# Optimization experiments

Hardware: AMD Instinct MI355X
Metric: run time of the kernel (lower is better)

The kernel has to match this reference:

```python
import jax, jax.numpy as jnp
import numpy as np

N_UU_LAYERS = 2
N_II_LAYERS = 2
ALPHA = 0.5
BETA = 0.5


def _sym_norm(edge_index, n):
    # PyG gcn_norm without self loops: norm = deg^-1/2[row] * deg^-1/2[col]
    row, col = edge_index[0], edge_index[1]
    deg = jax.ops.segment_sum(jnp.ones(row.shape, jnp.float32), col, num_segments=n)
    dinv = jnp.where(deg > 0, jax.lax.rsqrt(jnp.maximum(deg, 1e-12)), 0.0)
    return dinv[row] * dinv[col]


def _propagate(x, edge_index, norm, n):
    # gather from source, weight by norm, scatter-sum into target
    row, col = edge_index[0], edge_index[1]
    return jax.ops.segment_sum(norm[:, None] * x[row], col, num_segments=n)


def setup_inputs() -> dict:
    key = jax.random.key(0)
    ks = jax.random.split(key, 16)
    U, I, D, R, S = 50000, 50000, 64, 5, 2
    E_REL, E_SIM, B = 1000000, 1600000, 8192
    sc = 0.1  # xavier-ish scale for d=64
    return {
        "Gu": jax.random.normal(ks[0], (U, D), jnp.float32) * sc,
        "Gi": jax.random.normal(ks[1], (I, D), jnp.float32) * sc,
        "Gus": jax.random.normal(ks[2], (U, D), jnp.float32) * sc,
        "Gis": jax.random.normal(ks[3], (I, D), jnp.float32) * sc,
        "W_conv": jax.random.normal(ks[4], (R, D, D), jnp.float32) * sc,
        "W_dense": jax.random.normal(ks[5], (D, D), jnp.float32) * sc,
        "P": jax.random.normal(ks[6], (S, D, D), jnp.float32) * sc,
        "A": jax.random.uniform(ks[7], (R, S), jnp.float32),
        "relations": jnp.arange(1, R + 1, dtype=jnp.float32),
        "edge_index_rel": jax.random.randint(ks[8], (R, 2, E_REL), 0, U + I, jnp.int32),
        "edge_index_uu": jax.random.randint(ks[9], (2, E_SIM), 0, U, jnp.int32),
        "edge_index_ii": jax.random.randint(ks[10], (2, E_SIM), 0, I, jnp.int32),
        "user": jax.random.randint(ks[11], (B,), 0, U, jnp.int32),
        "item": jax.random.randint(ks[12], (B,), 0, I, jnp.int32),
    }


def reference(Gu, Gi, Gus, Gis, W_conv, W_dense, P, A, relations,
              edge_index_rel, edge_index_uu, edge_index_ii, user, item):
    U, I = Gu.shape[0], Gi.shape[0]
    N = U + I
    R = W_conv.shape[0]

    # LGConv stacks on user-user and item-item similarity graphs
    norm_uu = _sym_norm(edge_index_uu, U)
    gus = Gus
    for _ in range(N_UU_LAYERS):
        gus = _propagate(gus, edge_index_uu, norm_uu, U)
    norm_ii = _sym_norm(edge_index_ii, I)
    gis = Gis
    for _ in range(N_II_LAYERS):
        gis = _propagate(gis, edge_index_ii, norm_ii, I)

    # Per-relation GCNConv (1 layer, linear-then-aggregate, ReLU), sum accumulation
    x0 = jnp.concatenate([Gu, Gi], axis=0)  # [N, D]
    acc = jnp.zeros((N, W_conv.shape[2]), x0.dtype)
    for r in range(R):
        ei = edge_index_rel[r]
        norm = _sym_norm(ei, N)
        xr = x0 @ W_conv[r]
        xr = jax.nn.relu(_propagate(xr, ei, norm, N))
        acc = acc + xr

    emb = acc @ W_dense  # dense layer, no bias; dropout p=0
    zu, zi = emb[:U], emb[U:]

    # batch gather and blend with similarity-propagated embeddings
    gu = (1.0 - ALPHA) * zu[user] + ALPHA * gus[user]
    gi_b = (1.0 - BETA) * zi[item] + BETA * gis[item]

    # basis-weighted bilinear scoring per relation
    Q = jnp.einsum('rs,sde->rde', A, P)             # [R, D, D]
    pui = jnp.einsum('bd,rde,be->br', gu, Q, gi_b)  # [B, R]
    xui = jnp.sum(relations * jax.nn.softmax(pui, axis=1), axis=1)
    return (xui, pui)
```

## Files before the change

kernel.cpp:

```cpp
#include <hip/hip_runtime.h>
#include <hip/hip_bf16.h>

#define DD 64
#define C_REL 40
#define C_SIM 80

static inline int cdiv(long long a, long long b) { return (int)((a + b - 1) / b); }


__global__ void k_scatter_pad(const int* __restrict__ row, const int* __restrict__ col, int E,
                              int* __restrict__ cnt, int* __restrict__ edp, int C) {
    int e = blockIdx.x * blockDim.x + threadIdx.x;
    if (e >= E) return;
    int r = row[e], c = col[e];
    int pos = atomicAdd(&cnt[c], 1);
    if (pos < C) edp[(size_t)c * C + pos] = r;
}

__global__ void k_scatter_rel(const int* __restrict__ row, const int* __restrict__ col, int E,
                              int* __restrict__ cnt, int* __restrict__ edp, int C,
                              const unsigned char* __restrict__ sel) {
    int e = blockIdx.x * blockDim.x + threadIdx.x;
    if (e >= E) return;
    int r = row[e], c = col[e];
    int pos = atomicAdd(&cnt[c], 1);
    if (sel[c] && pos < C) edp[(size_t)c * C + pos] = r;
}

__global__ void k_mark(unsigned char* __restrict__ sel, const int* __restrict__ user,
                       const int* __restrict__ item, int B, int U) {
    int t = blockIdx.x * blockDim.x + threadIdx.x;
    if (t >= 2 * B) return;
    int node = (t < B) ? user[t] : (U + item[t - B]);
    sel[node] = 1;
}

__global__ void k_dinv_i(const int* __restrict__ cnt, float* __restrict__ dinv, int n) {
    int i = blockIdx.x * blockDim.x + threadIdx.x;
    if (i < n) { int d = cnt[i]; dinv[i] = d > 0 ? rsqrtf((float)d) : 0.f; }
}


__global__ __launch_bounds__(256) void k_gather_pad(const float* __restrict__ src, float* __restrict__ dst,
                                                    const int* __restrict__ edp, const int* __restrict__ cnt,
                                                    const float* __restrict__ dinv, int C, int nNodes) {
    int t = blockIdx.x * blockDim.x + threadIdx.x;
    int node = t >> 4;
    if (node >= nNodes) return;
    int k4 = (t & 15) << 2;
    int deg = cnt[node]; if (deg > C) deg = C;
    float dc = dinv[node];
    const int* lst = edp + (size_t)node * C;
    float4 acc = make_float4(0.f, 0.f, 0.f, 0.f);
    for (int e = 0; e < deg; ++e) {
        int rs = lst[e];
        float nn = dc * dinv[rs];
        float4 v = *(const float4*)(src + (size_t)rs * DD + k4);
        acc.x += nn * v.x; acc.y += nn * v.y; acc.z += nn * v.z; acc.w += nn * v.w;
    }
    *(float4*)(dst + (size_t)node * DD + k4) = acc;
}

__global__ __launch_bounds__(256) void k_gather_sel_sim(const float* __restrict__ src, float* __restrict__ dst,
                                                        const int* __restrict__ edp, const int* __restrict__ cnt,
                                                        const float* __restrict__ dinv, int C,
                                                        const int* __restrict__ idx, int B) {
    int t = blockIdx.x * blockDim.x + threadIdx.x;
    int j = t >> 4;
    if (j >= B) return;
    int k4 = (t & 15) << 2;
    int node = idx[j];
    int deg = cnt[node]; if (deg > C) deg = C;
    float dc = dinv[node];
    const int* lst = edp + (size_t)node * C;
    float4 acc = make_float4(0.f, 0.f, 0.f, 0.f);
    for (int e = 0; e < deg; ++e) {
        int rs = lst[e];
        float nn = dc * dinv[rs];
        float4 v = *(const float4*)(src + (size_t)rs * DD + k4);
        acc.x += nn * v.x; acc.y += nn * v.y; acc.z += nn * v.z; acc.w += nn * v.w;
    }
    *(float4*)(dst + (size_t)j * DD + k4) = acc;
}

__global__ __launch_bounds__(256) void k_gather_x0_rel(const float* __restrict__ Gu, const float* __restrict__ Gi,
                                                       int U, float* __restrict__ TMP,
                                                       const int* __restrict__ edp, const int* __restrict__ cnt,
                                                       int C, const int* __restrict__ user,
                                                       const int* __restrict__ item, int B) {
    int t = blockIdx.x * blockDim.x + threadIdx.x;
    int j = t >> 4;
    if (j >= 2 * B) return;
    int k4 = (t & 15) << 2;
    int node = (j < B) ? user[j] : (U + item[j - B]);
    int cn = cnt[node];
    int deg = cn > C ? C : cn;
    float dc = cn > 0 ? rsqrtf((float)cn) : 0.f;
    const int* lst = edp + (size_t)node * C;
    float4 acc = make_float4(0.f, 0.f, 0.f, 0.f);
    for (int e = 0; e < deg; ++e) {
        int rs = lst[e];
        int cr = cnt[rs];
        float nn = dc * (cr > 0 ? rsqrtf((float)cr) : 0.f);
        const float* srow = (rs < U) ? (Gu + (size_t)rs * DD) : (Gi + (size_t)(rs - U) * DD);
        float4 v = *(const float4*)(srow + k4);
        acc.x += nn * v.x; acc.y += nn * v.y; acc.z += nn * v.z; acc.w += nn * v.w;
    }
    *(float4*)(TMP + (size_t)j * DD + k4) = acc;
}


template <bool RELU_ACC>
__global__ __launch_bounds__(256) void k_matmul64t(const float* __restrict__ X, const float* __restrict__ W,
                                                   float* __restrict__ out, int Nrows) {
    __shared__ float Wl[64 * 64];
    int tid = threadIdx.x;
    for (int t = tid; t < 1024; t += 256) ((float4*)Wl)[t] = ((const float4*)W)[t];
    __syncthreads();
    int row = blockIdx.x * 64 + (tid >> 2);
    if (row >= Nrows) return;
    const float* xs = X + (size_t)row * DD;
    int j0 = (tid & 3) << 4;
    float acc[16];
#pragma unroll
    for (int j = 0; j < 16; ++j) acc[j] = 0.f;
#pragma unroll 4
    for (int k = 0; k < 64; k += 4) {
        float4 xv = *(const float4*)(xs + k);
        const float* w0 = Wl + k * 64 + j0;
#pragma unroll
        for (int j = 0; j < 16; ++j) acc[j] += xv.x * w0[j];
#pragma unroll
        for (int j = 0; j < 16; ++j) acc[j] += xv.y * w0[64 + j];
#pragma unroll
        for (int j = 0; j < 16; ++j) acc[j] += xv.z * w0[128 + j];
#pragma unroll
        for (int j = 0; j < 16; ++j) acc[j] += xv.w * w0[192 + j];
    }
    float* o = out + (size_t)row * DD + j0;
    if (RELU_ACC) {
#pragma unroll
        for (int j = 0; j < 4; ++j) {
            float4 cur = ((float4*)o)[j];
            cur.x += fmaxf(acc[4 * j + 0], 0.f);
            cur.y += fmaxf(acc[4 * j + 1], 0.f);
            cur.z += fmaxf(acc[4 * j + 2], 0.f);
            cur.w += fmaxf(acc[4 * j + 3], 0.f);
            ((float4*)o)[j] = cur;
        }
    } else {
#pragma unroll
        for (int j = 0; j < 4; ++j)
            ((float4*)o)[j] = make_float4(acc[4 * j], acc[4 * j + 1], acc[4 * j + 2], acc[4 * j + 3]);
    }
}

__global__ void k_blend(const float* __restrict__ gus_sel, const float* __restrict__ gis_sel,
                        const float* __restrict__ EMB, float* __restrict__ gu, float* __restrict__ gi,
                        int B) {
    int t = blockIdx.x * blockDim.x + threadIdx.x;
    if (t >= 2 * B * 16) return;
    int j = t >> 4, k = t & 15;
    float4 e = ((const float4*)(EMB + (size_t)j * DD))[k];
    if (j < B) {
        float4 s = ((const float4*)(gus_sel + (size_t)j * DD))[k];
        ((float4*)(gu + (size_t)j * DD))[k] =
            make_float4(0.5f * (s.x + e.x), 0.5f * (s.y + e.y), 0.5f * (s.z + e.z), 0.5f * (s.w + e.w));
    } else {
        int jj = j - B;
        float4 s = ((const float4*)(gis_sel + (size_t)jj * DD))[k];
        ((float4*)(gi + (size_t)jj * DD))[k] =
            make_float4(0.5f * (s.x + e.x), 0.5f * (s.y + e.y), 0.5f * (s.z + e.z), 0.5f * (s.w + e.w));
    }
}

__global__ void k_build_Q(const float* __restrict__ A, const float* __restrict__ P,
                          float* __restrict__ Q, int R, int S) {
    int t = blockIdx.x * blockDim.x + threadIdx.x;
    if (t >= R * 4096) return;
    int r = t / 4096, de = t % 4096;
    float acc = 0.f;
    for (int s = 0; s < S; ++s) acc += A[r * S + s] * P[(size_t)s * 4096 + de];
    Q[t] = acc;
}

__global__ __launch_bounds__(256) void k_pui2(const float* __restrict__ gu, const float* __restrict__ gi,
                                              const float* __restrict__ Q, float* __restrict__ pout,
                                              int B, int R) {
    int wid = (int)(((long long)blockIdx.x * blockDim.x + threadIdx.x) >> 6);
    int lane = threadIdx.x & 63;
    if (wid >= B * R) return;
    int b = wid / R, r = wid % R;
    const float* Qr = Q + (size_t)r * 4096;
    float gu_l = gu[(size_t)b * DD + lane];
    float gi_l = gi[(size_t)b * DD + lane];
    float acc = 0.f;
#pragma unroll 8
    for (int d = 0; d < 64; ++d) {
        float gud = __shfl(gu_l, d, 64);
        acc += gud * Qr[d * 64 + lane];
    }
    acc *= gi_l;
#pragma unroll
    for (int off = 32; off > 0; off >>= 1) acc += __shfl_down(acc, off, 64);
    if (lane == 0) pout[wid] = acc;
}

__global__ void k_softmax_out(const float* __restrict__ pui, const float* __restrict__ rel,
                              float* __restrict__ xui, int B, int R) {
    int b = blockIdx.x * blockDim.x + threadIdx.x;
    if (b >= B) return;
    float m = -1e30f;
    for (int r = 0; r < R; ++r) m = fmaxf(m, pui[(size_t)b * R + r]);
    float se = 0.f, sw = 0.f;
    for (int r = 0; r < R; ++r) {
        float e = expf(pui[(size_t)b * R + r] - m);
        se += e; sw += rel[r] * e;
    }
    xui[b] = sw / se;
}

extern "C" void kernel_launch(void* const* d_in, const int* in_sizes, int n_in,
                              void* d_out, int out_size, void* d_ws, size_t ws_size,
                              hipStream_t stream) {
    const float* Gu      = (const float*)d_in[0];
    const float* Gi      = (const float*)d_in[1];
    const float* Gus     = (const float*)d_in[2];
    const float* Gis     = (const float*)d_in[3];
    const float* W_conv  = (const float*)d_in[4];
    const float* W_dense = (const float*)d_in[5];
    const float* P       = (const float*)d_in[6];
    const float* A       = (const float*)d_in[7];
    const float* rel     = (const float*)d_in[8];
    const int*   ei_rel  = (const int*)d_in[9];
    const int*   ei_uu   = (const int*)d_in[10];
    const int*   ei_ii   = (const int*)d_in[11];
    const int*   user    = (const int*)d_in[12];
    const int*   item    = (const int*)d_in[13];

    const int U = in_sizes[0] / DD;
    const int I = in_sizes[1] / DD;
    const int N = U + I;
    const int R = in_sizes[8];
    const int S = in_sizes[6] / 4096;
    const int E_REL = in_sizes[9] / (2 * R);
    const int E_SIM = in_sizes[10] / 2;
    const int B = in_sizes[12];
    const size_t RN = (size_t)R * N;

    size_t edpElems = (size_t)U * C_SIM;
    if ((size_t)I * C_SIM > edpElems) edpElems = (size_t)I * C_SIM;
    if ((size_t)N * C_REL > edpElems) edpElems = (size_t)N * C_REL;
    edpElems = (edpElems + 3) & ~(size_t)3;

    int maxUI = U > I ? U : I;

    char* p = (char*)d_ws;
    int*   edp     = (int*)p;   p += edpElems * 4;
    int*   cnt     = (int*)p;   p += RN * 4;
    float* dinv    = (float*)p; p += (size_t)(U + I) * 4;
    unsigned char* sel = (unsigned char*)p; p += ((size_t)N + 15) & ~(size_t)15;
    float* gus_sel = (float*)p; p += (size_t)B * DD * 4;
    float* gis_sel = (float*)p; p += (size_t)B * DD * 4;
    float* ACC     = (float*)p; p += (size_t)2 * B * DD * 4;
    float* TMP     = (float*)p; p += (size_t)2 * B * DD * 4;
    float* EMB     = (float*)p; p += (size_t)2 * B * DD * 4;
    float* gu      = (float*)p; p += (size_t)B * DD * 4;
    float* gi      = (float*)p; p += (size_t)B * DD * 4;
    float* Q       = (float*)p; p += (size_t)R * 4096 * 4;
    float* BIG0    = (float*)p; p += (size_t)maxUI * DD * 4;

    float* xui = (float*)d_out;
    float* pui = (float*)d_out + B;

    const int BT = 256;

    hipMemsetAsync(cnt, 0, (size_t)(U + I) * 4, stream);
    k_scatter_pad<<<cdiv(E_SIM, BT), BT, 0, stream>>>(ei_uu, ei_uu + E_SIM, E_SIM, cnt, edp, C_SIM);
    k_dinv_i<<<cdiv(U, BT), BT, 0, stream>>>(cnt, dinv, U);
    k_gather_pad<<<cdiv((long long)U * 16, BT), BT, 0, stream>>>(Gus, BIG0, edp, cnt, dinv, C_SIM, U);
    k_gather_sel_sim<<<cdiv((long long)B * 16, BT), BT, 0, stream>>>(BIG0, gus_sel, edp, cnt, dinv, C_SIM, user, B);
    k_scatter_pad<<<cdiv(E_SIM, BT), BT, 0, stream>>>(ei_ii, ei_ii + E_SIM, E_SIM, cnt + U, edp, C_SIM);
    k_dinv_i<<<cdiv(I, BT), BT, 0, stream>>>(cnt + U, dinv + U, I);
    k_gather_pad<<<cdiv((long long)I * 16, BT), BT, 0, stream>>>(Gis, BIG0, edp, cnt + U, dinv + U, C_SIM, I);
    k_gather_sel_sim<<<cdiv((long long)B * 16, BT), BT, 0, stream>>>(BIG0, gis_sel, edp, cnt + U, dinv + U, C_SIM, item, B);

    hipMemsetAsync(cnt, 0, RN * 4, stream);
    hipMemsetAsync(sel, 0, (size_t)N, stream);
    hipMemsetAsync(ACC, 0, (size_t)2 * B * DD * 4, stream);
    k_mark<<<cdiv(2 * B, BT), BT, 0, stream>>>(sel, user, item, B, U);
    for (int r = 0; r < R; ++r) {
        const int* rrow = ei_rel + (size_t)r * 2 * E_REL;
        const int* rcol = rrow + E_REL;
        k_scatter_rel<<<cdiv(E_REL, BT), BT, 0, stream>>>(rrow, rcol, E_REL, cnt + (size_t)r * N, edp, C_REL, sel);
        k_gather_x0_rel<<<cdiv((long long)2 * B * 16, BT), BT, 0, stream>>>(Gu, Gi, U, TMP, edp,
                                                                            cnt + (size_t)r * N, C_REL,
                                                                            user, item, B);
        k_matmul64t<true><<<cdiv(2 * B, 64), BT, 0, stream>>>(TMP, W_conv + (size_t)r * 4096, ACC, 2 * B);
    }

    k_matmul64t<false><<<cdiv(2 * B, 64), BT, 0, stream>>>(ACC, W_dense, EMB, 2 * B);
    k_blend<<<cdiv((long long)2 * B * 16, BT), BT, 0, stream>>>(gus_sel, gis_sel, EMB, gu, gi, B);

    k_build_Q<<<cdiv((long long)R * 4096, BT), BT, 0, stream>>>(A, P, Q, R, S);
    k_pui2<<<cdiv((long long)B * R * 64, BT), BT, 0, stream>>>(gu, gi, Q, pui, B, R);
    k_softmax_out<<<cdiv(B, BT), BT, 0, stream>>>(pui, rel, xui, B, R);
}
```

Baseline: 958.1 us.

## Merge user/item similarity passes, use 16-bit padded adjacency, split relation histogram

```diff
diff --git a/kernel.cpp b/kernel.cpp
--- a/kernel.cpp
+++ b/kernel.cpp
@@ -7,24 +7,112 @@
 
 static inline int cdiv(long long a, long long b) { return (int)((a + b - 1) / b); }
 
-
-__global__ void k_scatter_pad(const int* __restrict__ row, const int* __restrict__ col, int E,
-                              int* __restrict__ cnt, int* __restrict__ edp, int C) {
-    int e = blockIdx.x * blockDim.x + threadIdx.x;
-    if (e >= E) return;
-    int r = row[e], c = col[e];
-    int pos = atomicAdd(&cnt[c], 1);
-    if (pos < C) edp[(size_t)c * C + pos] = r;
-}
-
-__global__ void k_scatter_rel(const int* __restrict__ row, const int* __restrict__ col, int E,
-                              int* __restrict__ cnt, int* __restrict__ edp, int C,
-                              const unsigned char* __restrict__ sel) {
-    int e = blockIdx.x * blockDim.x + threadIdx.x;
-    if (e >= E) return;
-    int r = row[e], c = col[e];
-    int pos = atomicAdd(&cnt[c], 1);
-    if (sel[c] && pos < C) edp[(size_t)c * C + pos] = r;
+__global__ void k_scatter_sim16(const int* __restrict__ rowU, const int* __restrict__ colU,
+                                const int* __restrict__ rowI, const int* __restrict__ colI,
+                                int E, int U, int* __restrict__ cnt,
+                                unsigned short* __restrict__ edpU, unsigned short* __restrict__ edpI) {
+    long long t = (long long)blockIdx.x * blockDim.x + threadIdx.x;
+    if (t >= 2LL * E) return;
+    if (t < E) {
+        int r = rowU[t], c = colU[t];
+        int pos = atomicAdd(&cnt[c], 1);
+        if (pos < C_SIM) edpU[(size_t)c * C_SIM + pos] = (unsigned short)r;
+    } else {
+        int e = (int)(t - E);
+        int r = rowI[e], c = colI[e];
+        int pos = atomicAdd(&cnt[U + c], 1);
+        if (pos < C_SIM) edpI[(size_t)c * C_SIM + pos] = (unsigned short)r;
+    }
+}
+
+__global__ void k_dinv_i(const int* __restrict__ cnt, float* __restrict__ dinv, int n) {
+    int i = blockIdx.x * blockDim.x + threadIdx.x;
+    if (i < n) { int d = cnt[i]; dinv[i] = d > 0 ? rsqrtf((float)d) : 0.f; }
+}
+
+__global__ __launch_bounds__(256) void k_gather_sim1(const float* __restrict__ Gus, const float* __restrict__ Gis,
+                                                     int U, int UI, float* __restrict__ H1,
+                                                     const unsigned short* __restrict__ edpU,
+                                                     const unsigned short* __restrict__ edpI,
+                                                     const int* __restrict__ cnt, const float* __restrict__ dinv) {
+    int t = blockIdx.x * blockDim.x + threadIdx.x;
+    int node = t >> 4;
+    if (node >= UI) return;
+    int k4 = (t & 15) << 2;
+    int deg = cnt[node]; if (deg > C_SIM) deg = C_SIM;
+    float dc = dinv[node];
+    float4 acc = make_float4(0.f, 0.f, 0.f, 0.f);
+    if (node < U) {
+        const unsigned short* lst = edpU + (size_t)node * C_SIM;
+        for (int e = 0; e < deg; ++e) {
+            int rs = lst[e];
+            float nn = dc * dinv[rs];
+            float4 v = *(const float4*)(Gus + (size_t)rs * DD + k4);
+            acc.x += nn * v.x; acc.y += nn * v.y; acc.z += nn * v.z; acc.w += nn * v.w;
+        }
+    } else {
+        int loc = node - U;
+        const unsigned short* lst = edpI + (size_t)loc * C_SIM;
+        for (int e = 0; e < deg; ++e) {
+            int rs = lst[e];
+            float nn = dc * dinv[U + rs];
+            float4 v = *(const float4*)(Gis + (size_t)rs * DD + k4);
+            acc.x += nn * v.x; acc.y += nn * v.y; acc.z += nn * v.z; acc.w += nn * v.w;
+        }
+    }
+    *(float4*)(H1 + (size_t)node * DD + k4) = acc;
+}
+
+__global__ __launch_bounds__(256) void k_gather_sim2(const float* __restrict__ H1, int U,
+                                                     float* __restrict__ SEL2,
+                                                     const unsigned short* __restrict__ edpU,
+                                                     const unsigned short* __restrict__ edpI,
+                                                     const int* __restrict__ cnt, const float* __restrict__ dinv,
+                                                     const int* __restrict__ user, const int* __restrict__ item,
+                                                     int B) {
+    int t = blockIdx.x * blockDim.x + threadIdx.x;
+    int j = t >> 4;
+    if (j >= 2 * B) return;
+    int k4 = (t & 15) << 2;
+    float4 acc = make_float4(0.f, 0.f, 0.f, 0.f);
+    if (j < B) {
+        int node = user[j];
+        int deg = cnt[node]; if (deg > C_SIM) deg = C_SIM;
+        float dc = dinv[node];
+        const unsigned short* lst = edpU + (size_t)node * C_SIM;
+        for (int e = 0; e < deg; ++e) {
+            int rs = lst[e];
+            float nn = dc * dinv[rs];
+            float4 v = *(const float4*)(H1 + (size_t)rs * DD + k4);
+            acc.x += nn * v.x; acc.y += nn * v.y; acc.z += nn * v.z; acc.w += nn * v.w;
+        }
+    } else {
+        int loc = item[j - B];
+        int deg = cnt[U + loc]; if (deg > C_SIM) deg = C_SIM;
+        float dc = dinv[U + loc];
+        const unsigned short* lst = edpI + (size_t)loc * C_SIM;
+        for (int e = 0; e < deg; ++e) {
+            int rs = lst[e];
+            float nn = dc * dinv[U + rs];
+            float4 v = *(const float4*)(H1 + (size_t)(U + rs) * DD + k4);
+            acc.x += nn * v.x; acc.y += nn * v.y; acc.z += nn * v.z; acc.w += nn * v.w;
+        }
+    }
+    *(float4*)(SEL2 + (size_t)j * DD + k4) = acc;
+}
+
+
+__global__ void k_hist_rel(const int* __restrict__ ei_rel, int E, int N, int R,
+                           int* __restrict__ cntRel) {
+    long long total = (long long)R * E;
+    long long t = (long long)blockIdx.x * blockDim.x + threadIdx.x;
+    long long stride = (long long)gridDim.x * blockDim.x;
+    for (; t < total; t += stride) {
+        int r = (int)(t / E);
+        int e = (int)(t - (long long)r * E);
+        int c = ei_rel[(size_t)r * 2 * E + E + e];
+        atomicAdd(&cntRel[(size_t)r * N + c], 1);
+    }
 }
 
 __global__ void k_mark(unsigned char* __restrict__ sel, const int* __restrict__ user,
@@ -35,58 +123,21 @@
     sel[node] = 1;
 }
 
-__global__ void k_dinv_i(const int* __restrict__ cnt, float* __restrict__ dinv, int n) {
-    int i = blockIdx.x * blockDim.x + threadIdx.x;
-    if (i < n) { int d = cnt[i]; dinv[i] = d > 0 ? rsqrtf((float)d) : 0.f; }
-}
-
-
-__global__ __launch_bounds__(256) void k_gather_pad(const float* __restrict__ src, float* __restrict__ dst,
-                                                    const int* __restrict__ edp, const int* __restrict__ cnt,
-                                                    const float* __restrict__ dinv, int C, int nNodes) {
-    int t = blockIdx.x * blockDim.x + threadIdx.x;
-    int node = t >> 4;
-    if (node >= nNodes) return;
-    int k4 = (t & 15) << 2;
-    int deg = cnt[node]; if (deg > C) deg = C;
-    float dc = dinv[node];
-    const int* lst = edp + (size_t)node * C;
-    float4 acc = make_float4(0.f, 0.f, 0.f, 0.f);
-    for (int e = 0; e < deg; ++e) {
-        int rs = lst[e];
-        float nn = dc * dinv[rs];
-        float4 v = *(const float4*)(src + (size_t)rs * DD + k4);
-        acc.x += nn * v.x; acc.y += nn * v.y; acc.z += nn * v.z; acc.w += nn * v.w;
-    }
-    *(float4*)(dst + (size_t)node * DD + k4) = acc;
-}
-
-__global__ __launch_bounds__(256) void k_gather_sel_sim(const float* __restrict__ src, float* __restrict__ dst,
-                                                        const int* __restrict__ edp, const int* __restrict__ cnt,
-                                                        const float* __restrict__ dinv, int C,
-                                                        const int* __restrict__ idx, int B) {
-    int t = blockIdx.x * blockDim.x + threadIdx.x;
-    int j = t >> 4;
-    if (j >= B) return;
-    int k4 = (t & 15) << 2;
-    int node = idx[j];
-    int deg = cnt[node]; if (deg > C) deg = C;
-    float dc = dinv[node];
-    const int* lst = edp + (size_t)node * C;
-    float4 acc = make_float4(0.f, 0.f, 0.f, 0.f);
-    for (int e = 0; e < deg; ++e) {
-        int rs = lst[e];
-        float nn = dc * dinv[rs];
-        float4 v = *(const float4*)(src + (size_t)rs * DD + k4);
-        acc.x += nn * v.x; acc.y += nn * v.y; acc.z += nn * v.z; acc.w += nn * v.w;
-    }
-    *(float4*)(dst + (size_t)j * DD + k4) = acc;
+__global__ void k_scatter_rel_f(const int* __restrict__ row, const int* __restrict__ col, int E,
+                                const unsigned char* __restrict__ sel, int* __restrict__ cur,
+                                int* __restrict__ edp) {
+    int e = blockIdx.x * blockDim.x + threadIdx.x;
+    if (e >= E) return;
+    int c = col[e];
+    if (!sel[c]) return;
+    int pos = atomicAdd(&cur[c], 1);
+    if (pos < C_REL) edp[(size_t)c * C_REL + pos] = row[e];
 }
 
 __global__ __launch_bounds__(256) void k_gather_x0_rel(const float* __restrict__ Gu, const float* __restrict__ Gi,
                                                        int U, float* __restrict__ TMP,
                                                        const int* __restrict__ edp, const int* __restrict__ cnt,
-                                                       int C, const int* __restrict__ user,
+                                                       const int* __restrict__ user,
                                                        const int* __restrict__ item, int B) {
     int t = blockIdx.x * blockDim.x + threadIdx.x;
     int j = t >> 4;
@@ -94,9 +145,9 @@
     int k4 = (t & 15) << 2;
     int node = (j < B) ? user[j] : (U + item[j - B]);
     int cn = cnt[node];
-    int deg = cn > C ? C : cn;
+    int deg = cn > C_REL ? C_REL : cn;
     float dc = cn > 0 ? rsqrtf((float)cn) : 0.f;
-    const int* lst = edp + (size_t)node * C;
+    const int* lst = edp + (size_t)node * C_REL;
     float4 acc = make_float4(0.f, 0.f, 0.f, 0.f);
     for (int e = 0; e < deg; ++e) {
         int rs = lst[e];
@@ -155,23 +206,16 @@
     }
 }
 
-__global__ void k_blend(const float* __restrict__ gus_sel, const float* __restrict__ gis_sel,
-                        const float* __restrict__ EMB, float* __restrict__ gu, float* __restrict__ gi,
-                        int B) {
+__global__ void k_blend(const float* __restrict__ SEL2, const float* __restrict__ EMB,
+                        float* __restrict__ gu, float* __restrict__ gi, int B) {
     int t = blockIdx.x * blockDim.x + threadIdx.x;
     if (t >= 2 * B * 16) return;
     int j = t >> 4, k = t & 15;
     float4 e = ((const float4*)(EMB + (size_t)j * DD))[k];
-    if (j < B) {
-        float4 s = ((const float4*)(gus_sel + (size_t)j * DD))[k];
-        ((float4*)(gu + (size_t)j * DD))[k] =
-            make_float4(0.5f * (s.x + e.x), 0.5f * (s.y + e.y), 0.5f * (s.z + e.z), 0.5f * (s.w + e.w));
-    } else {
-        int jj = j - B;
-        float4 s = ((const float4*)(gis_sel + (size_t)jj * DD))[k];
-        ((float4*)(gi + (size_t)jj * DD))[k] =
-            make_float4(0.5f * (s.x + e.x), 0.5f * (s.y + e.y), 0.5f * (s.z + e.z), 0.5f * (s.w + e.w));
-    }
+    float4 s = ((const float4*)(SEL2 + (size_t)j * DD))[k];
+    float4 o = make_float4(0.5f * (s.x + e.x), 0.5f * (s.y + e.y), 0.5f * (s.z + e.z), 0.5f * (s.w + e.w));
+    if (j < B) ((float4*)(gu + (size_t)j * DD))[k] = o;
+    else       ((float4*)(gi + (size_t)(j - B) * DD))[k] = o;
 }
 
 __global__ void k_build_Q(const float* __restrict__ A, const float* __restrict__ P,
@@ -248,59 +292,57 @@
     const int B = in_sizes[12];
     const size_t RN = (size_t)R * N;
 
-    size_t edpElems = (size_t)U * C_SIM;
-    if ((size_t)I * C_SIM > edpElems) edpElems = (size_t)I * C_SIM;
-    if ((size_t)N * C_REL > edpElems) edpElems = (size_t)N * C_REL;
-    edpElems = (edpElems + 3) & ~(size_t)3;
-
-    int maxUI = U > I ? U : I;
-
     char* p = (char*)d_ws;
-    int*   edp     = (int*)p;   p += edpElems * 4;
-    int*   cnt     = (int*)p;   p += RN * 4;
-    float* dinv    = (float*)p; p += (size_t)(U + I) * 4;
+    unsigned short* edpU = (unsigned short*)p; p += (((size_t)U * C_SIM * 2 + 15) & ~(size_t)15);
+    unsigned short* edpI = (unsigned short*)p; p += (((size_t)I * C_SIM * 2 + 15) & ~(size_t)15);
+    int*   edpR    = (int*)p;   p += (size_t)N * C_REL * 4;
+    int*   cntSim  = (int*)p;   p += (size_t)N * 4;
+    int*   cntRel  = (int*)p;   p += RN * 4;
+    int*   curRel  = (int*)p;   p += RN * 4;
+    float* dinv    = (float*)p; p += (size_t)N * 4;
     unsigned char* sel = (unsigned char*)p; p += ((size_t)N + 15) & ~(size_t)15;
-    float* gus_sel = (float*)p; p += (size_t)B * DD * 4;
-    float* gis_sel = (float*)p; p += (size_t)B * DD * 4;
+    float* SEL2    = (float*)p; p += (size_t)2 * B * DD * 4;
     float* ACC     = (float*)p; p += (size_t)2 * B * DD * 4;
     float* TMP     = (float*)p; p += (size_t)2 * B * DD * 4;
     float* EMB     = (float*)p; p += (size_t)2 * B * DD * 4;
     float* gu      = (float*)p; p += (size_t)B * DD * 4;
     float* gi      = (float*)p; p += (size_t)B * DD * 4;
     float* Q       = (float*)p; p += (size_t)R * 4096 * 4;
-    float* BIG0    = (float*)p; p += (size_t)maxUI * DD * 4;
+    float* H1      = (float*)p; p += (size_t)N * DD * 4;
 
     float* xui = (float*)d_out;
     float* pui = (float*)d_out + B;
 
     const int BT = 256;
 
-    hipMemsetAsync(cnt, 0, (size_t)(U + I) * 4, stream);
-    k_scatter_pad<<<cdiv(E_SIM, BT), BT, 0, stream>>>(ei_uu, ei_uu + E_SIM, E_SIM, cnt, edp, C_SIM);
-    k_dinv_i<<<cdiv(U, BT), BT, 0, stream>>>(cnt, dinv, U);
-    k_gather_pad<<<cdiv((long long)U * 16, BT), BT, 0, stream>>>(Gus, BIG0, edp, cnt, dinv, C_SIM, U);
-    k_gather_sel_sim<<<cdiv((long long)B * 16, BT), BT, 0, stream>>>(BIG0, gus_sel, edp, cnt, dinv, C_SIM, user, B);
-    k_scatter_pad<<<cdiv(E_SIM, BT), BT, 0, stream>>>(ei_ii, ei_ii + E_SIM, E_SIM, cnt + U, edp, C_SIM);
-    k_dinv_i<<<cdiv(I, BT), BT, 0, stream>>>(cnt + U, dinv + U, I);
-    k_gather_pad<<<cdiv((long long)I * 16, BT), BT, 0, stream>>>(Gis, BIG0, edp, cnt + U, dinv + U, C_SIM, I);
-    k_gather_sel_sim<<<cdiv((long long)B * 16, BT), BT, 0, stream>>>(BIG0, gis_sel, edp, cnt + U, dinv + U, C_SIM, item, B);
-
-    hipMemsetAsync(cnt, 0, RN * 4, stream);
+    hipMemsetAsync(cntSim, 0, (size_t)N * 4, stream);
+    k_scatter_sim16<<<cdiv(2LL * E_SIM, BT), BT, 0, stream>>>(ei_uu, ei_uu + E_SIM, ei_ii, ei_ii + E_SIM,
+                                                              E_SIM, U, cntSim, edpU, edpI);
+    k_dinv_i<<<cdiv(N, BT), BT, 0, stream>>>(cntSim, dinv, N);
+    k_gather_sim1<<<cdiv((long long)N * 16, BT), BT, 0, stream>>>(Gus, Gis, U, N, H1, edpU, edpI, cntSim, dinv);
+    k_gather_sim2<<<cdiv((long long)2 * B * 16, BT), BT, 0, stream>>>(H1, U, SEL2, edpU, edpI, cntSim, dinv,
+                                                                      user, item, B);
+
+    hipMemsetAsync(cntRel, 0, RN * 4, stream);
+    hipMemsetAsync(curRel, 0, RN * 4, stream);
     hipMemsetAsync(sel, 0, (size_t)N, stream);
     hipMemsetAsync(ACC, 0, (size_t)2 * B * DD * 4, stream);
     k_mark<<<cdiv(2 * B, BT), BT, 0, stream>>>(sel, user, item, B, U);
+    {
+        int hgrid = cdiv((long long)R * E_REL, BT); if (hgrid > 8192) hgrid = 8192;
+        k_hist_rel<<<hgrid, BT, 0, stream>>>(ei_rel, E_REL, N, R, cntRel);
+    }
     for (int r = 0; r < R; ++r) {
         const int* rrow = ei_rel + (size_t)r * 2 * E_REL;
         const int* rcol = rrow + E_REL;
-        k_scatter_rel<<<cdiv(E_REL, BT), BT, 0, stream>>>(rrow, rcol, E_REL, cnt + (size_t)r * N, edp, C_REL, sel);
-        k_gather_x0_rel<<<cdiv((long long)2 * B * 16, BT), BT, 0, stream>>>(Gu, Gi, U, TMP, edp,
-                                                                            cnt + (size_t)r * N, C_REL,
-                                                                            user, item, B);
+        k_scatter_rel_f<<<cdiv(E_REL, BT), BT, 0, stream>>>(rrow, rcol, E_REL, sel, curRel + (size_t)r * N, edpR);
+        k_gather_x0_rel<<<cdiv((long long)2 * B * 16, BT), BT, 0, stream>>>(Gu, Gi, U, TMP, edpR,
+                                                                            cntRel + (size_t)r * N, user, item, B);
         k_matmul64t<true><<<cdiv(2 * B, 64), BT, 0, stream>>>(TMP, W_conv + (size_t)r * 4096, ACC, 2 * B);
     }
 
     k_matmul64t<false><<<cdiv(2 * B, 64), BT, 0, stream>>>(ACC, W_dense, EMB, 2 * B);
-    k_blend<<<cdiv((long long)2 * B * 16, BT), BT, 0, stream>>>(gus_sel, gis_sel, EMB, gu, gi, B);
+    k_blend<<<cdiv((long long)2 * B * 16, BT), BT, 0, stream>>>(SEL2, EMB, gu, gi, B);
 
     k_build_Q<<<cdiv((long long)R * 4096, BT), BT, 0, stream>>>(A, P, Q, R, S);
     k_pui2<<<cdiv((long long)B * R * 64, BT), BT, 0, stream>>>(gu, gi, Q, pui, B, R);
```

Result: slower. 1.025 ms (+7.0%).

## Build similarity-graph adjacency per node slice in LDS with 16-bit indices

Applied to the files above, without the earlier changes.

```diff
diff --git a/kernel.cpp b/kernel.cpp
--- a/kernel.cpp
+++ b/kernel.cpp
@@ -4,53 +4,74 @@
 #define DD 64
 #define C_REL 40
 #define C_SIM 80
+#define SLICE 512
 
 static inline int cdiv(long long a, long long b) { return (int)((a + b - 1) / b); }
 
-
-__global__ void k_scatter_pad(const int* __restrict__ row, const int* __restrict__ col, int E,
-                              int* __restrict__ cnt, int* __restrict__ edp, int C) {
-    int e = blockIdx.x * blockDim.x + threadIdx.x;
-    if (e >= E) return;
-    int r = row[e], c = col[e];
-    int pos = atomicAdd(&cnt[c], 1);
-    if (pos < C) edp[(size_t)c * C + pos] = r;
-}
-
-__global__ void k_scatter_rel(const int* __restrict__ row, const int* __restrict__ col, int E,
-                              int* __restrict__ cnt, int* __restrict__ edp, int C,
-                              const unsigned char* __restrict__ sel) {
-    int e = blockIdx.x * blockDim.x + threadIdx.x;
-    if (e >= E) return;
-    int r = row[e], c = col[e];
-    int pos = atomicAdd(&cnt[c], 1);
-    if (sel[c] && pos < C) edp[(size_t)c * C + pos] = r;
-}
-
-__global__ void k_mark(unsigned char* __restrict__ sel, const int* __restrict__ user,
-                       const int* __restrict__ item, int B, int U) {
-    int t = blockIdx.x * blockDim.x + threadIdx.x;
-    if (t >= 2 * B) return;
-    int node = (t < B) ? user[t] : (U + item[t - B]);
-    sel[node] = 1;
-}
-
-__global__ void k_dinv_i(const int* __restrict__ cnt, float* __restrict__ dinv, int n) {
-    int i = blockIdx.x * blockDim.x + threadIdx.x;
-    if (i < n) { int d = cnt[i]; dinv[i] = d > 0 ? rsqrtf((float)d) : 0.f; }
+__global__ __launch_bounds__(256) void k_build_sim(const int* __restrict__ eiU, const int* __restrict__ eiI,
+                                                   int E, int U, int I, int nsU,
+                                                   int* __restrict__ cnt, float* __restrict__ dinv,
+                                                   unsigned short* __restrict__ edpU,
+                                                   unsigned short* __restrict__ edpI) {
+    extern __shared__ char smem[];
+    int* cnt_s = (int*)smem;
+    unsigned short* slots_s = (unsigned short*)(smem + SLICE * 4);
+    int tid = threadIdx.x;
+    bool isU = (int)blockIdx.x < nsU;
+    int sl = isU ? blockIdx.x : blockIdx.x - nsU;
+    int n = isU ? U : I;
+    int lo = sl * SLICE;
+    int len = n - lo; if (len > SLICE) len = SLICE;
+    if (len <= 0) return;
+    const int* row = isU ? eiU : eiI;
+    const int* col = row + E;
+
+    for (int i = tid; i < len; i += 256) cnt_s[i] = 0;
+    __syncthreads();
+
+    if (((E & 3) == 0) && ((((size_t)col) & 15) == 0)) {
+        for (int e = tid * 4; e + 3 < E; e += 1024) {
+            int4 c4 = *(const int4*)(col + e);
+            unsigned l0 = (unsigned)(c4.x - lo), l1 = (unsigned)(c4.y - lo);
+            unsigned l2 = (unsigned)(c4.z - lo), l3 = (unsigned)(c4.w - lo);
+            if (l0 < (unsigned)len) { int pos = atomicAdd(&cnt_s[l0], 1); if (pos < C_SIM) slots_s[l0 * C_SIM + pos] = (unsigned short)row[e]; }
+            if (l1 < (unsigned)len) { int pos = atomicAdd(&cnt_s[l1], 1); if (pos < C_SIM) slots_s[l1 * C_SIM + pos] = (unsigned short)row[e + 1]; }
+            if (l2 < (unsigned)len) { int pos = atomicAdd(&cnt_s[l2], 1); if (pos < C_SIM) slots_s[l2 * C_SIM + pos] = (unsigned short)row[e + 2]; }
+            if (l3 < (unsigned)len) { int pos = atomicAdd(&cnt_s[l3], 1); if (pos < C_SIM) slots_s[l3 * C_SIM + pos] = (unsigned short)row[e + 3]; }
+        }
+    } else {
+        for (int e = tid; e < E; e += 256) {
+            unsigned l = (unsigned)(col[e] - lo);
+            if (l < (unsigned)len) { int pos = atomicAdd(&cnt_s[l], 1); if (pos < C_SIM) slots_s[l * C_SIM + pos] = (unsigned short)row[e]; }
+        }
+    }
+    __syncthreads();
+
+    int goff = (isU ? 0 : U) + lo;
+    for (int i = tid; i < len; i += 256) {
+        int d = cnt_s[i];
+        cnt[goff + i] = d;
+        dinv[goff + i] = d > 0 ? rsqrtf((float)d) : 0.f;
+    }
+    unsigned short* dst = (isU ? edpU : edpI) + (size_t)lo * C_SIM;
+    int n16 = len * C_SIM / 8;
+    const uint4* s4 = (const uint4*)slots_s;
+    uint4* d4 = (uint4*)dst;
+    for (int i = tid; i < n16; i += 256) d4[i] = s4[i];
 }
 
 
 __global__ __launch_bounds__(256) void k_gather_pad(const float* __restrict__ src, float* __restrict__ dst,
-                                                    const int* __restrict__ edp, const int* __restrict__ cnt,
-                                                    const float* __restrict__ dinv, int C, int nNodes) {
+                                                    const unsigned short* __restrict__ edp,
+                                                    const int* __restrict__ cnt,
+                                                    const float* __restrict__ dinv, int nNodes) {
     int t = blockIdx.x * blockDim.x + threadIdx.x;
     int node = t >> 4;
     if (node >= nNodes) return;
     int k4 = (t & 15) << 2;
-    int deg = cnt[node]; if (deg > C) deg = C;
+    int deg = cnt[node]; if (deg > C_SIM) deg = C_SIM;
     float dc = dinv[node];
-    const int* lst = edp + (size_t)node * C;
+    const unsigned short* lst = edp + (size_t)node * C_SIM;
     float4 acc = make_float4(0.f, 0.f, 0.f, 0.f);
     for (int e = 0; e < deg; ++e) {
         int rs = lst[e];
@@ -62,17 +83,18 @@
 }
 
 __global__ __launch_bounds__(256) void k_gather_sel_sim(const float* __restrict__ src, float* __restrict__ dst,
-                                                        const int* __restrict__ edp, const int* __restrict__ cnt,
-                                                        const float* __restrict__ dinv, int C,
+                                                        const unsigned short* __restrict__ edp,
+                                                        const int* __restrict__ cnt,
+                                                        const float* __restrict__ dinv,
                                                         const int* __restrict__ idx, int B) {
     int t = blockIdx.x * blockDim.x + threadIdx.x;
     int j = t >> 4;
     if (j >= B) return;
     int k4 = (t & 15) << 2;
     int node = idx[j];
-    int deg = cnt[node]; if (deg > C) deg = C;
+    int deg = cnt[node]; if (deg > C_SIM) deg = C_SIM;
     float dc = dinv[node];
-    const int* lst = edp + (size_t)node * C;
+    const unsigned short* lst = edp + (size_t)node * C_SIM;
     float4 acc = make_float4(0.f, 0.f, 0.f, 0.f);
     for (int e = 0; e < deg; ++e) {
         int rs = lst[e];
@@ -83,10 +105,29 @@
     *(float4*)(dst + (size_t)j * DD + k4) = acc;
 }
 
+
+__global__ void k_mark(unsigned char* __restrict__ sel, const int* __restrict__ user,
+                       const int* __restrict__ item, int B, int U) {
+    int t = blockIdx.x * blockDim.x + threadIdx.x;
+    if (t >= 2 * B) return;
+    int node = (t < B) ? user[t] : (U + item[t - B]);
+    sel[node] = 1;
+}
+
+__global__ void k_scatter_rel(const int* __restrict__ row, const int* __restrict__ col, int E,
+                              int* __restrict__ cnt, int* __restrict__ edp,
+                              const unsigned char* __restrict__ sel) {
+    int e = blockIdx.x * blockDim.x + threadIdx.x;
+    if (e >= E) return;
+    int r = row[e], c = col[e];
+    int pos = atomicAdd(&cnt[c], 1);
+    if (sel[c] && pos < C_REL) edp[(size_t)c * C_REL + pos] = r;
+}
+
 __global__ __launch_bounds__(256) void k_gather_x0_rel(const float* __restrict__ Gu, const float* __restrict__ Gi,
                                                        int U, float* __restrict__ TMP,
                                                        const int* __restrict__ edp, const int* __restrict__ cnt,
-                                                       int C, const int* __restrict__ user,
+                                                       const int* __restrict__ user,
                                                        const int* __restrict__ item, int B) {
     int t = blockIdx.x * blockDim.x + threadIdx.x;
     int j = t >> 4;
@@ -94,9 +135,9 @@
     int k4 = (t & 15) << 2;
     int node = (j < B) ? user[j] : (U + item[j - B]);
     int cn = cnt[node];
-    int deg = cn > C ? C : cn;
+    int deg = cn > C_REL ? C_REL : cn;
     float dc = cn > 0 ? rsqrtf((float)cn) : 0.f;
-    const int* lst = edp + (size_t)node * C;
+    const int* lst = edp + (size_t)node * C_REL;
     float4 acc = make_float4(0.f, 0.f, 0.f, 0.f);
     for (int e = 0; e < deg; ++e) {
         int rs = lst[e];
@@ -247,18 +288,15 @@
     const int E_SIM = in_sizes[10] / 2;
     const int B = in_sizes[12];
     const size_t RN = (size_t)R * N;
-
-    size_t edpElems = (size_t)U * C_SIM;
-    if ((size_t)I * C_SIM > edpElems) edpElems = (size_t)I * C_SIM;
-    if ((size_t)N * C_REL > edpElems) edpElems = (size_t)N * C_REL;
-    edpElems = (edpElems + 3) & ~(size_t)3;
-
-    int maxUI = U > I ? U : I;
+    const int maxUI = U > I ? U : I;
 
     char* p = (char*)d_ws;
-    int*   edp     = (int*)p;   p += edpElems * 4;
-    int*   cnt     = (int*)p;   p += RN * 4;
-    float* dinv    = (float*)p; p += (size_t)(U + I) * 4;
+    unsigned short* edpU = (unsigned short*)p; p += (((size_t)U * C_SIM * 2 + 15) & ~(size_t)15);
+    unsigned short* edpI = (unsigned short*)p; p += (((size_t)I * C_SIM * 2 + 15) & ~(size_t)15);
+    int*   edpR    = (int*)p;   p += (size_t)N * C_REL * 4;
+    int*   cntSim  = (int*)p;   p += (size_t)N * 4;
+    int*   cntRel  = (int*)p;   p += RN * 4;
+    float* dinv    = (float*)p; p += (size_t)N * 4;
     unsigned char* sel = (unsigned char*)p; p += ((size_t)N + 15) & ~(size_t)15;
     float* gus_sel = (float*)p; p += (size_t)B * DD * 4;
     float* gis_sel = (float*)p; p += (size_t)B * DD * 4;
@@ -275,27 +313,27 @@
 
     const int BT = 256;
 
-    hipMemsetAsync(cnt, 0, (size_t)(U + I) * 4, stream);
-    k_scatter_pad<<<cdiv(E_SIM, BT), BT, 0, stream>>>(ei_uu, ei_uu + E_SIM, E_SIM, cnt, edp, C_SIM);
-    k_dinv_i<<<cdiv(U, BT), BT, 0, stream>>>(cnt, dinv, U);
-    k_gather_pad<<<cdiv((long long)U * 16, BT), BT, 0, stream>>>(Gus, BIG0, edp, cnt, dinv, C_SIM, U);
-    k_gather_sel_sim<<<cdiv((long long)B * 16, BT), BT, 0, stream>>>(BIG0, gus_sel, edp, cnt, dinv, C_SIM, user, B);
-    k_scatter_pad<<<cdiv(E_SIM, BT), BT, 0, stream>>>(ei_ii, ei_ii + E_SIM, E_SIM, cnt + U, edp, C_SIM);
-    k_dinv_i<<<cdiv(I, BT), BT, 0, stream>>>(cnt + U, dinv + U, I);
-    k_gather_pad<<<cdiv((long long)I * 16, BT), BT, 0, stream>>>(Gis, BIG0, edp, cnt + U, dinv + U, C_SIM, I);
-    k_gather_sel_sim<<<cdiv((long long)B * 16, BT), BT, 0, stream>>>(BIG0, gis_sel, edp, cnt + U, dinv + U, C_SIM, item, B);
-
-    hipMemsetAsync(cnt, 0, RN * 4, stream);
+    {
+        int nsU = cdiv(U, SLICE), nsI = cdiv(I, SLICE);
+        size_t lds = (size_t)SLICE * 4 + (size_t)SLICE * C_SIM * 2;
+        k_build_sim<<<nsU + nsI, BT, lds, stream>>>(ei_uu, ei_ii, E_SIM, U, I, nsU,
+                                                    cntSim, dinv, edpU, edpI);
+    }
+    k_gather_pad<<<cdiv((long long)U * 16, BT), BT, 0, stream>>>(Gus, BIG0, edpU, cntSim, dinv, U);
+    k_gather_sel_sim<<<cdiv((long long)B * 16, BT), BT, 0, stream>>>(BIG0, gus_sel, edpU, cntSim, dinv, user, B);
+    k_gather_pad<<<cdiv((long long)I * 16, BT), BT, 0, stream>>>(Gis, BIG0, edpI, cntSim + U, dinv + U, I);
+    k_gather_sel_sim<<<cdiv((long long)B * 16, BT), BT, 0, stream>>>(BIG0, gis_sel, edpI, cntSim + U, dinv + U, item, B);
+
+    hipMemsetAsync(cntRel, 0, RN * 4, stream);
     hipMemsetAsync(sel, 0, (size_t)N, stream);
     hipMemsetAsync(ACC, 0, (size_t)2 * B * DD * 4, stream);
     k_mark<<<cdiv(2 * B, BT), BT, 0, stream>>>(sel, user, item, B, U);
     for (int r = 0; r < R; ++r) {
         const int* rrow = ei_rel + (size_t)r * 2 * E_REL;
         const int* rcol = rrow + E_REL;
-        k_scatter_rel<<<cdiv(E_REL, BT), BT, 0, stream>>>(rrow, rcol, E_REL, cnt + (size_t)r * N, edp, C_REL, sel);
-        k_gather_x0_rel<<<cdiv((long long)2 * B * 16, BT), BT, 0, stream>>>(Gu, Gi, U, TMP, edp,
-                                                                            cnt + (size_t)r * N, C_REL,
-                                                                            user, item, B);
+        k_scatter_rel<<<cdiv(E_REL, BT), BT, 0, stream>>>(rrow, rcol, E_REL, cntRel + (size_t)r * N, edpR, sel);
+        k_gather_x0_rel<<<cdiv((long long)2 * B * 16, BT), BT, 0, stream>>>(Gu, Gi, U, TMP, edpR,
+                                                                            cntRel + (size_t)r * N, user, item, B);
         k_matmul64t<true><<<cdiv(2 * B, 64), BT, 0, stream>>>(TMP, W_conv + (size_t)r * 4096, ACC, 2 * B);
     }
 
```

After: 1.830 ms. 91.0% more time.
